# Kernel optimization log

Measured on AMD Instinct MI355X. Metric: run time of the kernel, lower is better.

Reference implementation:

```python
import math
import jax, jax.numpy as jnp
import numpy as np

B, T, D, H, L = 8, 2048, 1024, 16, 4
DK = D // H
EPS_LN = 1e-5
EPS_ATTN = 1e-6


def setup_inputs() -> dict:
    key = jax.random.key(0)
    ks = jax.random.split(key, 8)
    w = lambda k, shape: jax.random.normal(k, shape, dtype=jnp.float32) * 0.02
    return {
        'x_in': jax.random.normal(ks[0], (B, T, D), dtype=jnp.float32),
        'Wq': w(ks[1], (L, D, D)), 'bq': jnp.zeros((L, D), jnp.float32),
        'Wk': w(ks[2], (L, D, D)), 'bk': jnp.zeros((L, D), jnp.float32),
        'Wv': w(ks[3], (L, D, D)), 'bv': jnp.zeros((L, D), jnp.float32),
        'Wo': w(ks[4], (L, D, D)), 'bo': jnp.zeros((L, D), jnp.float32),
        'W1': w(ks[5], (L, D, 4 * D)), 'b1': jnp.zeros((L, 4 * D), jnp.float32),
        'W2': w(ks[6], (L, 4 * D, D)), 'b2': jnp.zeros((L, D), jnp.float32),
        'ln1_s': jnp.ones((L, D), jnp.float32), 'ln1_b': jnp.zeros((L, D), jnp.float32),
        'ln2_s': jnp.ones((L, D), jnp.float32), 'ln2_b': jnp.zeros((L, D), jnp.float32),
        'lnf_s': jnp.ones((D,), jnp.float32), 'lnf_b': jnp.zeros((D,), jnp.float32),
    }


def _layernorm(x, scale, bias):
    mu = jnp.mean(x, axis=-1, keepdims=True)
    var = jnp.mean(jnp.square(x - mu), axis=-1, keepdims=True)
    return (x - mu) * jax.lax.rsqrt(var + EPS_LN) * scale + bias


def _sinusoidal_pos_emb(t, d):
    # fairseq/MulT-style: sin half then cos half, positions start at 1 (padding_idx+1)
    half = d // 2
    freq = jnp.exp(jnp.arange(half, dtype=jnp.float32) * (-math.log(10000.0) / (half - 1)))
    pos = (jnp.arange(t, dtype=jnp.float32) + 1.0)[:, None] * freq[None, :]  # (T, half)
    return jnp.concatenate([jnp.sin(pos), jnp.cos(pos)], axis=-1)  # (T, D)


def _linear_attention(q, k, v):
    # q,k,v: (B, T, H, DK). elu+1 feature map, non-causal linear attention.
    qp = jax.nn.elu(q) + 1.0
    kp = jax.nn.elu(k) + 1.0
    kv = jnp.einsum('bshd,bshm->bhmd', kp, v)          # (B, H, DK_v, DK)
    ksum = jnp.sum(kp, axis=1)                          # (B, H, DK)
    z = 1.0 / (jnp.einsum('blhd,bhd->blh', qp, ksum) + EPS_ATTN)
    return jnp.einsum('blhd,bhmd,blh->blhm', qp, kv, z)  # (B, T, H, DK)


def _encoder_layer(x, Wq, bq, Wk, bk, Wv, bv, Wo, bo, W1, b1, W2, b2, ln1_s, ln1_b, ln2_s, ln2_b):
    b, t, d = x.shape
    # pre-LN self-attention block
    h = _layernorm(x, ln1_s, ln1_b)
    q = (h @ Wq + bq).reshape(b, t, H, DK)
    k = (h @ Wk + bk).reshape(b, t, H, DK)
    v = (h @ Wv + bv).reshape(b, t, H, DK)
    attn = _linear_attention(q, k, v).reshape(b, t, d)
    x = x + (attn @ Wo + bo)
    # pre-LN FFN block
    h = _layernorm(x, ln2_s, ln2_b)
    h = jax.nn.relu(h @ W1 + b1) @ W2 + b2
    return x + h


def reference(x_in, Wq, bq, Wk, bk, Wv, bv, Wo, bo, W1, b1, W2, b2,
              ln1_s, ln1_b, ln2_s, ln2_b, lnf_s, lnf_b):
    b, t, d = x_in.shape
    x = math.sqrt(d) * x_in + _sinusoidal_pos_emb(t, d)[None, :, :]
    for i in range(L):
        x = _encoder_layer(x, Wq[i], bq[i], Wk[i], bk[i], Wv[i], bv[i], Wo[i], bo[i],
                           W1[i], b1[i], W2[i], b2[i], ln1_s[i], ln1_b[i], ln2_s[i], ln2_b[i])
    return _layernorm(x, lnf_s, lnf_b)
```

## Files before the change

### kernel.cpp

```cpp
#include <hip/hip_runtime.h>
#include <cstdint>

#define BSZ   8
#define TSEQ  2048
#define DMOD  1024
#define NROWS 16384
#define NHEAD 16
#define DHEAD 64

__device__ __forceinline__ float bf2f(unsigned short h) {
  union { unsigned int u; float f; } a; a.u = ((unsigned int)h) << 16; return a.f;
}
__device__ __forceinline__ unsigned short f2bf(float f) {
  union { float f; unsigned int u; } a; a.f = f;
  unsigned int u = a.u;
  u += 0x7fffu + ((u >> 16) & 1u);
  return (unsigned short)(u >> 16);
}

typedef __bf16 bf16x8 __attribute__((ext_vector_type(8)));
typedef float  f32x4  __attribute__((ext_vector_type(4)));

typedef const __attribute__((address_space(1))) void* gas_ptr;
typedef __attribute__((address_space(3))) void*       las_ptr;

__device__ __forceinline__ void gl_lds16(const void* g, void* l) {
  __builtin_amdgcn_global_load_lds((gas_ptr)g, (las_ptr)l, 16, 0, 0);
}

__global__ __launch_bounds__(256) void transpose_cvt(const float* __restrict__ src,
                                                     unsigned short* __restrict__ dst,
                                                     int K, int N) {
  __shared__ float tile[32][33];
  const int n0 = blockIdx.x * 32, k0 = blockIdx.y * 32;
  const int tx = threadIdx.x, ty = threadIdx.y;
#pragma unroll
  for (int r = 0; r < 4; ++r)
    tile[ty + r * 8][tx] = src[(size_t)(k0 + ty + r * 8) * N + n0 + tx];
  __syncthreads();
#pragma unroll
  for (int r = 0; r < 4; ++r)
    dst[(size_t)(n0 + ty + r * 8) * K + k0 + tx] = f2bf(tile[tx][ty + r * 8]);
}

__global__ __launch_bounds__(256) void concat_bias(const float* __restrict__ bq,
                                                   const float* __restrict__ bk,
                                                   const float* __restrict__ bv,
                                                   float* __restrict__ out) {
  int i = blockIdx.x * 256 + threadIdx.x;
  int l = i / 3072, c = i - l * 3072;
  float v;
  if (c < 1024)       v = bq[l * 1024 + c];
  else if (c < 2048)  v = bk[l * 1024 + c - 1024];
  else                v = bv[l * 1024 + c - 2048];
  out[i] = v;
}

__global__ __launch_bounds__(256) void embed_k(const float* __restrict__ xin,
                                               float* __restrict__ x) {
  const size_t row = blockIdx.x;
  const int t = blockIdx.x & (TSEQ - 1);
  const int tid = threadIdx.x;
  const int c = tid * 4;
  float4 xv = ((const float4*)(xin + row * DMOD))[tid];
  float o[4];
  float xs[4] = { xv.x, xv.y, xv.z, xv.w };
#pragma unroll
  for (int j = 0; j < 4; ++j) {
    int dd = c + j;
    int i = dd & 511;
    float fr = expf(-0.0180241494559221f * (float)i);
    float ang = (float)(t + 1) * fr;
    float pe = (dd < 512) ? sinf(ang) : cosf(ang);
    o[j] = 32.0f * xs[j] + pe;
  }
  float4 ov = { o[0], o[1], o[2], o[3] };
  ((float4*)(x + row * DMOD))[tid] = ov;
}

__global__ __launch_bounds__(256) void ln_k(const float* __restrict__ x,
                                            const float* __restrict__ gam,
                                            const float* __restrict__ bet,
                                            unsigned short* __restrict__ outH) {
  const int row = blockIdx.x;
  const int tid = threadIdx.x;
  const float4 xv = ((const float4*)(x + (size_t)row * DMOD))[tid];
  float sum = xv.x + xv.y + xv.z + xv.w;
  float sq  = xv.x * xv.x + xv.y * xv.y + xv.z * xv.z + xv.w * xv.w;
#pragma unroll
  for (int o = 32; o; o >>= 1) { sum += __shfl_xor(sum, o); sq += __shfl_xor(sq, o); }
  __shared__ float s1[4], s2[4];
  const int wid = tid >> 6, lane = tid & 63;
  if (lane == 0) { s1[wid] = sum; s2[wid] = sq; }
  __syncthreads();
  sum = s1[0] + s1[1] + s1[2] + s1[3];
  sq  = s2[0] + s2[1] + s2[2] + s2[3];
  const float mu = sum * (1.0f / 1024.0f);
  const float var = sq * (1.0f / 1024.0f) - mu * mu;
  const float rs = rsqrtf(var + 1e-5f);
  const float4 g = ((const float4*)gam)[tid];
  const float4 b = ((const float4*)bet)[tid];
  union { unsigned short s[4]; uint2 u; } p;
  p.s[0] = f2bf((xv.x - mu) * rs * g.x + b.x);
  p.s[1] = f2bf((xv.y - mu) * rs * g.y + b.y);
  p.s[2] = f2bf((xv.z - mu) * rs * g.z + b.z);
  p.s[3] = f2bf((xv.w - mu) * rs * g.w + b.w);
  ((uint2*)(outH + (size_t)row * DMOD))[tid] = p.u;
}

template <int FINAL>
__global__ __launch_bounds__(256) void addln_k(float* __restrict__ x,
                                               const unsigned short* y,
                                               const float* __restrict__ gam,
                                               const float* __restrict__ bet,
                                               unsigned short* outH, float* outF) {
  const int row = blockIdx.x;
  const int tid = threadIdx.x;
  float4 xv = ((const float4*)(x + (size_t)row * DMOD))[tid];
  union { uint2 u; unsigned short s[4]; } yv;
  yv.u = ((const uint2*)(y + (size_t)row * DMOD))[tid];
  xv.x += bf2f(yv.s[0]); xv.y += bf2f(yv.s[1]);
  xv.z += bf2f(yv.s[2]); xv.w += bf2f(yv.s[3]);
  float sum = xv.x + xv.y + xv.z + xv.w;
  float sq  = xv.x * xv.x + xv.y * xv.y + xv.z * xv.z + xv.w * xv.w;
#pragma unroll
  for (int o = 32; o; o >>= 1) { sum += __shfl_xor(sum, o); sq += __shfl_xor(sq, o); }
  __shared__ float s1[4], s2[4];
  const int wid = tid >> 6, lane = tid & 63;
  if (lane == 0) { s1[wid] = sum; s2[wid] = sq; }
  __syncthreads();
  sum = s1[0] + s1[1] + s1[2] + s1[3];
  sq  = s2[0] + s2[1] + s2[2] + s2[3];
  const float mu = sum * (1.0f / 1024.0f);
  const float var = sq * (1.0f / 1024.0f) - mu * mu;
  const float rs = rsqrtf(var + 1e-5f);
  const float4 g = ((const float4*)gam)[tid];
  const float4 b = ((const float4*)bet)[tid];
  float o0 = (xv.x - mu) * rs * g.x + b.x;
  float o1 = (xv.y - mu) * rs * g.y + b.y;
  float o2 = (xv.z - mu) * rs * g.z + b.z;
  float o3 = (xv.w - mu) * rs * g.w + b.w;
  if (FINAL) {
    float4 ov = { o0, o1, o2, o3 };
    ((float4*)(outF + (size_t)row * DMOD))[tid] = ov;
  } else {
    ((float4*)(x + (size_t)row * DMOD))[tid] = xv;
    union { unsigned short s[4]; uint2 u; } p;
    p.s[0] = f2bf(o0); p.s[1] = f2bf(o1); p.s[2] = f2bf(o2); p.s[3] = f2bf(o3);
    ((uint2*)(outH + (size_t)row * DMOD))[tid] = p.u;
  }
}

template <int RELU>
__global__ __launch_bounds__(256) void gemm_bt(const unsigned short* __restrict__ A,
                                               const unsigned short* __restrict__ Bt,
                                               const float* __restrict__ bias,
                                               unsigned short* __restrict__ outH,
                                               int M, int N, int K, int lda) {
  __shared__ __align__(16) unsigned short sm[16384];
  unsigned short* As = sm;
  unsigned short* Bs = sm + 8192;
  const int tid = threadIdx.x;
  const int wid = tid >> 6, lane = tid & 63;
  const int wm = wid >> 1, wn = wid & 1;
  const long m0 = (long)blockIdx.x * 128, n0 = (long)blockIdx.y * 128;

  f32x4 acc[4][4] = {};

  const int srow = tid >> 3;
  const int cswz = (tid & 7) ^ (srow & 7);
  const unsigned short* Ag = A + (size_t)(m0 + srow) * lda + cswz * 8;
  const unsigned short* Bg = Bt + (size_t)(n0 + srow) * K + cswz * 8;
  char* AsW = (char*)As + wid * 1024;
  char* BsW = (char*)Bs + wid * 1024;
  const size_t a32 = (size_t)32 * lda, b32 = (size_t)32 * K;

  const int fr = lane & 15;
  const int aswz = (((lane >> 4) ^ (lane & 7)) << 4);
  const int arow = (wm * 64 + fr) << 7;
  const int brow = (wn * 64 + fr) << 7;
  const char* smc = (const char*)sm;
  const char* smcB = (const char*)(sm + 8192);

  for (int kt = 0; kt < K; kt += 64) {
    __syncthreads();
#pragma unroll
    for (int p = 0; p < 4; ++p) {
      gl_lds16(Ag + kt + (size_t)p * a32, AsW + p * 4096);
      gl_lds16(Bg + kt + (size_t)p * b32, BsW + p * 4096);
    }
    __syncthreads();
#pragma unroll
    for (int s = 0; s < 2; ++s) {
      const int offs = aswz ^ (s << 6);
      bf16x8 af[4], bfv[4];
#pragma unroll
      for (int i = 0; i < 4; ++i) {
        af[i]  = *(const bf16x8*)(smc  + arow + i * 2048 + offs);
        bfv[i] = *(const bf16x8*)(smcB + brow + i * 2048 + offs);
      }
#pragma unroll
      for (int i = 0; i < 4; ++i)
#pragma unroll
        for (int j = 0; j < 4; ++j)
          acc[i][j] = __builtin_amdgcn_mfma_f32_16x16x32_bf16(af[i], bfv[j], acc[i][j], 0, 0, 0);
    }
  }

  const int cq = lane >> 4, cn = lane & 15;
#pragma unroll
  for (int p = 0; p < 2; ++p) {
    __syncthreads();
    if (wn == p) {
#pragma unroll
      for (int i = 0; i < 4; ++i)
#pragma unroll
        for (int j = 0; j < 4; ++j) {
          const float bb = bias[n0 + p * 64 + j * 16 + cn];
#pragma unroll
          for (int v = 0; v < 4; ++v) {
            float val = acc[i][j][v] + bb;
            if (RELU) val = fmaxf(val, 0.0f);
            sm[(wm * 64 + i * 16 + cq * 4 + v) * 72 + j * 16 + cn] = f2bf(val);
          }
        }
    }
    __syncthreads();
#pragma unroll
    for (int q = 0; q < 4; ++q) {
      const int idx = q * 256 + tid;
      const int row = idx >> 3, cc = idx & 7;
      uint4 valq = *(const uint4*)(sm + row * 72 + cc * 8);
      *(uint4*)(outH + (size_t)(m0 + row) * N + n0 + p * 64 + cc * 8) = valq;
    }
  }
}

__global__ __launch_bounds__(256) void attn_kv_partial(const unsigned short* __restrict__ qkv,
                                                       float* __restrict__ kvp,
                                                       float* __restrict__ ksump) {
  const int bh = blockIdx.x, tc = blockIdx.y;
  const int b = bh >> 4, h = bh & 15;
  const int tid = threadIdx.x;
  const int m = tid & 63, wid = tid >> 6;
  __shared__ float ks[32][64];
  __shared__ float vs[32][64];
  float acc[16];
#pragma unroll
  for (int j = 0; j < 16; ++j) acc[j] = 0.0f;
  float ksacc = 0.0f;
  const int tt = tid >> 3;
  const int dsb = (tid & 7) * 8;
  const size_t base = ((size_t)b * TSEQ + tc * 256) * 3072;
  const int kcol = 1024 + h * 64 + dsb, vcol = 2048 + h * 64 + dsb;
  for (int sc = 0; sc < 8; ++sc) {
    __syncthreads();
    const size_t roff = base + (size_t)(sc * 32 + tt) * 3072;
    uint4 kb = *(const uint4*)(qkv + roff + kcol);
    uint4 vb = *(const uint4*)(qkv + roff + vcol);
    const unsigned int* kw = (const unsigned int*)&kb;
    const unsigned int* vw = (const unsigned int*)&vb;
#pragma unroll
    for (int w2 = 0; w2 < 4; ++w2) {
      float k0 = bf2f((unsigned short)(kw[w2] & 0xffffu));
      float k1 = bf2f((unsigned short)(kw[w2] >> 16));
      ks[tt][dsb + 2 * w2]     = (k0 > 0.f) ? k0 + 1.f : expf(k0);
      ks[tt][dsb + 2 * w2 + 1] = (k1 > 0.f) ? k1 + 1.f : expf(k1);
      vs[tt][dsb + 2 * w2]     = bf2f((unsigned short)(vw[w2] & 0xffffu));
      vs[tt][dsb + 2 * w2 + 1] = bf2f((unsigned short)(vw[w2] >> 16));
    }
    __syncthreads();
#pragma unroll 4
    for (int t2 = 0; t2 < 32; ++t2) {
      float vv = vs[t2][m];
#pragma unroll
      for (int j = 0; j < 16; ++j) acc[j] += ks[t2][wid * 16 + j] * vv;
      if (tid < 64) ksacc += ks[t2][tid];
    }
  }
  float* dst = kvp + (size_t)(tc * 128 + bh) * 4096;
#pragma unroll
  for (int j = 0; j < 16; ++j) dst[(wid * 16 + j) * 64 + m] = acc[j];
  if (tid < 64) ksump[(size_t)(tc * 128 + bh) * 64 + tid] = ksacc;
}

__global__ __launch_bounds__(256) void attn_kv_reduce(const float* __restrict__ kvp,
                                                      const float* __restrict__ ksump,
                                                      float* __restrict__ kvf,
                                                      float* __restrict__ ksumf) {
  const int bh = blockIdx.x;
  const int tid = threadIdx.x;
  for (int i = tid; i < 4096; i += 256) {
    float s = 0.f;
#pragma unroll
    for (int tc = 0; tc < 8; ++tc) s += kvp[(size_t)(tc * 128 + bh) * 4096 + i];
    kvf[(size_t)bh * 4096 + i] = s;
  }
  if (tid < 64) {
    float s = 0.f;
#pragma unroll
    for (int tc = 0; tc < 8; ++tc) s += ksump[(size_t)(tc * 128 + bh) * 64 + tid];
    ksumf[bh * 64 + tid] = s;
  }
}

__global__ __launch_bounds__(256) void attn_out_k(const unsigned short* __restrict__ qkv,
                                                  const float* __restrict__ kvf,
                                                  const float* __restrict__ ksumf,
                                                  unsigned short* __restrict__ qkvO) {
  const int bh = blockIdx.x, tcb = blockIdx.y;
  const int b = bh >> 4, h = bh & 15;
  const int tid = threadIdx.x, wid = tid >> 6, lane = tid & 63;
  __shared__ float kvs[4096];
  __shared__ float kss[64];
  __shared__ float qps[4][64];
  for (int i = tid; i < 1024; i += 256)
    ((float4*)kvs)[i] = ((const float4*)(kvf + (size_t)bh * 4096))[i];
  if (tid < 64) kss[tid] = ksumf[bh * 64 + tid];
  __syncthreads();
  for (int it = 0; it < 64; ++it) {
    const int t = tcb * 256 + wid * 64 + it;
    const size_t row = (size_t)b * TSEQ + t;
    float q = bf2f(qkv[row * 3072 + h * 64 + lane]);
    float qp = (q > 0.f) ? q + 1.f : expf(q);
    float r = qp * kss[lane];
#pragma unroll
    for (int o = 32; o; o >>= 1) r += __shfl_xor(r, o);
    const float z = 1.0f / (r + 1e-6f);
    qps[wid][lane] = qp;
    float o = 0.f;
#pragma unroll
    for (int d = 0; d < 64; ++d) o += qps[wid][d] * kvs[d * 64 + lane];
    qkvO[row * 3072 + h * 64 + lane] = f2bf(o * z);
  }
}

extern "C" void kernel_launch(void* const* d_in, const int* in_sizes, int n_in,
                              void* d_out, int out_size, void* d_ws, size_t ws_size,
                              hipStream_t stream) {
  const float* x_in = (const float*)d_in[0];
  const float* Wq = (const float*)d_in[1];
  const float* bq = (const float*)d_in[2];
  const float* Wk = (const float*)d_in[3];
  const float* bk = (const float*)d_in[4];
  const float* Wv = (const float*)d_in[5];
  const float* bv = (const float*)d_in[6];
  const float* Wo = (const float*)d_in[7];
  const float* bo = (const float*)d_in[8];
  const float* W1 = (const float*)d_in[9];
  const float* b1 = (const float*)d_in[10];
  const float* W2 = (const float*)d_in[11];
  const float* b2 = (const float*)d_in[12];
  const float* ln1s = (const float*)d_in[13];
  const float* ln1b = (const float*)d_in[14];
  const float* ln2s = (const float*)d_in[15];
  const float* ln2b = (const float*)d_in[16];
  const float* lnfs = (const float*)d_in[17];
  const float* lnfb = (const float*)d_in[18];

  float* x = (float*)d_out;

  char* w = (char*)d_ws;
  unsigned short* hh    = (unsigned short*)(w + 0);
  unsigned short* qkv   = (unsigned short*)(w + 33554432);
  unsigned short* h1    = (unsigned short*)(w + 33554432);
  unsigned short* qkvwt = (unsigned short*)(w + 167772160);
  unsigned short* wot   = (unsigned short*)(w + 174063616);
  unsigned short* w1t   = (unsigned short*)(w + 176160768);
  unsigned short* w2t   = (unsigned short*)(w + 184549376);
  float*          bqkv  = (float*)(w + 192937984);
  float*          kvp   = (float*)(w + 192987136);
  float*          ksump = (float*)(w + 209764352);
  float*          kvf   = (float*)(w + 210026496);
  float*          ksumf = (float*)(w + 212123648);
  (void)ws_size; (void)in_sizes; (void)n_in; (void)out_size;

  dim3 b256(256);
  dim3 tb(32, 8);
  concat_bias<<<48, b256, 0, stream>>>(bq, bk, bv, bqkv);
  embed_k<<<NROWS, b256, 0, stream>>>(x_in, x);
  ln_k<<<NROWS, b256, 0, stream>>>(x, ln1s, ln1b, hh);

  for (int l = 0; l < 4; ++l) {
    transpose_cvt<<<dim3(32, 32), tb, 0, stream>>>(Wq + (size_t)l * 1048576, qkvwt,           1024, 1024);
    transpose_cvt<<<dim3(32, 32), tb, 0, stream>>>(Wk + (size_t)l * 1048576, qkvwt + 1048576, 1024, 1024);
    transpose_cvt<<<dim3(32, 32), tb, 0, stream>>>(Wv + (size_t)l * 1048576, qkvwt + 2097152, 1024, 1024);
    transpose_cvt<<<dim3(32, 32), tb, 0, stream>>>(Wo + (size_t)l * 1048576, wot, 1024, 1024);
    transpose_cvt<<<dim3(128, 32), tb, 0, stream>>>(W1 + (size_t)l * 4194304, w1t, 1024, 4096);
    transpose_cvt<<<dim3(32, 128), tb, 0, stream>>>(W2 + (size_t)l * 4194304, w2t, 4096, 1024);

    gemm_bt<0><<<dim3(128, 24), b256, 0, stream>>>(hh, qkvwt, bqkv + l * 3072, qkv,
                                                   NROWS, 3072, 1024, 1024);
    attn_kv_partial<<<dim3(128, 8), b256, 0, stream>>>(qkv, kvp, ksump);
    attn_kv_reduce<<<128, b256, 0, stream>>>(kvp, ksump, kvf, ksumf);
    attn_out_k<<<dim3(128, 8), b256, 0, stream>>>(qkv, kvf, ksumf, qkv);
    gemm_bt<0><<<dim3(128, 8), b256, 0, stream>>>(qkv, wot, bo + l * 1024, hh,
                                                  NROWS, 1024, 1024, 3072);
    addln_k<0><<<NROWS, b256, 0, stream>>>(x, hh, ln2s + l * 1024, ln2b + l * 1024, hh, nullptr);
    gemm_bt<1><<<dim3(128, 32), b256, 0, stream>>>(hh, w1t, b1 + l * 4096, h1,
                                                   NROWS, 4096, 1024, 1024);
    gemm_bt<0><<<dim3(128, 8), b256, 0, stream>>>(h1, w2t, b2 + l * 1024, hh,
                                                  NROWS, 1024, 4096, 4096);
    if (l < 3)
      addln_k<0><<<NROWS, b256, 0, stream>>>(x, hh, ln1s + (l + 1) * 1024, ln1b + (l + 1) * 1024,
                                             hh, nullptr);
    else
      addln_k<1><<<NROWS, b256, 0, stream>>>(x, hh, lnfs, lnfb, nullptr, x);
  }
}
```

Before: 3.411 ms.

## Replace 128x128 GEMM with 256x256 double-buffered 8-wave pipelined GEMM

Rewrites the bf16 GEMM to use 256x256 output tiles with 512 threads, double-buffered LDS staging and interleaved prefetch of next tiles between MFMA phases with wave priority hints. Adds an XCD-aware workgroup remap so neighbouring tiles share cache, and a swizzled LDS epilogue for coalesced stores. The aim is to raise MFMA utilisation and cut global memory traffic per FLOP, at the cost of 128KB LDS per block and high register pressure.

```diff
diff --git a/kernel.cpp b/kernel.cpp
--- a/kernel.cpp
+++ b/kernel.cpp
@@ -152,87 +152,181 @@
 }
 
 template <int RELU>
-__global__ __launch_bounds__(256) void gemm_bt(const unsigned short* __restrict__ A,
-                                               const unsigned short* __restrict__ Bt,
-                                               const float* __restrict__ bias,
-                                               unsigned short* __restrict__ outH,
-                                               int M, int N, int K, int lda) {
-  __shared__ __align__(16) unsigned short sm[16384];
-  unsigned short* As = sm;
-  unsigned short* Bs = sm + 8192;
+__global__ __launch_bounds__(512, 2) void gemm256(const unsigned short* __restrict__ A,
+                                                  const unsigned short* __restrict__ Bt,
+                                                  const float* __restrict__ bias,
+                                                  unsigned short* __restrict__ outH,
+                                                  int M, int N, int K, int lda) {
+  __shared__ __align__(16) unsigned short sm[65536];
   const int tid = threadIdx.x;
   const int wid = tid >> 6, lane = tid & 63;
-  const int wm = wid >> 1, wn = wid & 1;
-  const long m0 = (long)blockIdx.x * 128, n0 = (long)blockIdx.y * 128;
-
-  f32x4 acc[4][4] = {};
+  const int wm = wid >> 2, wn = wid & 3;
+
+  const int nwg = gridDim.x;
+  const int q = nwg >> 3, r = nwg & 7;
+  const int xcd = blockIdx.x & 7, sub = blockIdx.x >> 3;
+  const int wg = (xcd < r ? xcd * (q + 1) : r * (q + 1) + (xcd - r) * q) + sub;
+  const int nbm = M >> 8;
+  const int bm = wg % nbm, bn = wg / nbm;
+  const long m0 = (long)bm << 8, n0 = (long)bn << 8;
 
   const int srow = tid >> 3;
   const int cswz = (tid & 7) ^ (srow & 7);
   const unsigned short* Ag = A + (size_t)(m0 + srow) * lda + cswz * 8;
   const unsigned short* Bg = Bt + (size_t)(n0 + srow) * K + cswz * 8;
-  char* AsW = (char*)As + wid * 1024;
-  char* BsW = (char*)Bs + wid * 1024;
-  const size_t a32 = (size_t)32 * lda, b32 = (size_t)32 * K;
+  char* const smb = (char*)sm;
+  const int nT = K >> 6;
+
+#define STAGE_A(t, h)                                                              \
+  do {                                                                             \
+    const unsigned short* g_ = Ag + (size_t)(t) * 64 + (size_t)((h) * 128) * lda;  \
+    char* d_ = smb + (((t) & 1) << 15) + ((h) << 14) + (wid << 10);                \
+    gl_lds16(g_, d_);                                                              \
+    gl_lds16(g_ + ((size_t)lda << 6), d_ + 8192);                                  \
+  } while (0)
+#define STAGE_B(t, h)                                                              \
+  do {                                                                             \
+    const unsigned short* g_ = Bg + (size_t)(t) * 64 + (size_t)((h) * 128) * K;    \
+    char* d_ = smb + 65536 + (((t) & 1) << 15) + ((h) << 14) + (wid << 10);        \
+    gl_lds16(g_, d_);                                                              \
+    gl_lds16(g_ + ((size_t)K << 6), d_ + 8192);                                    \
+  } while (0)
 
   const int fr = lane & 15;
-  const int aswz = (((lane >> 4) ^ (lane & 7)) << 4);
-  const int arow = (wm * 64 + fr) << 7;
-  const int brow = (wn * 64 + fr) << 7;
-  const char* smc = (const char*)sm;
-  const char* smcB = (const char*)(sm + 8192);
-
-  for (int kt = 0; kt < K; kt += 64) {
-    __syncthreads();
-#pragma unroll
-    for (int p = 0; p < 4; ++p) {
-      gl_lds16(Ag + kt + (size_t)p * a32, AsW + p * 4096);
-      gl_lds16(Bg + kt + (size_t)p * b32, BsW + p * 4096);
+  const int aswz = ((lane >> 4) ^ (lane & 7)) << 4;
+  const int aoff = (wm * 128 + fr) * 128;
+  const int boff = (wn * 64 + fr) * 128;
+
+  f32x4 acc[8][4] = {};
+  bf16x8 a0[4][2], a1[4][2], bfr[4][2];
+
+  STAGE_A(0, 0); STAGE_A(0, 1); STAGE_B(0, 0); STAGE_B(0, 1);
+  if (nT > 1) {
+    STAGE_B(1, 1); STAGE_B(1, 0); STAGE_A(1, 1);
+    asm volatile("s_waitcnt vmcnt(6)" ::: "memory");
+  } else {
+    asm volatile("s_waitcnt vmcnt(0)" ::: "memory");
+  }
+  asm volatile("s_barrier" ::: "memory");
+
+  for (int T = 0; T < nT; ++T) {
+    const char* Ab = smb + ((T & 1) << 15);
+    const char* Bb = Ab + 65536;
+
+#pragma unroll
+    for (int i = 0; i < 4; ++i)
+#pragma unroll
+      for (int ks = 0; ks < 2; ++ks) {
+        a0[i][ks]  = *(const bf16x8*)(Ab + aoff + i * 2048 + (aswz ^ (ks << 6)));
+        bfr[i][ks] = *(const bf16x8*)(Bb + boff + i * 2048 + (aswz ^ (ks << 6)));
+      }
+    if (T + 1 < nT) STAGE_A(T + 1, 0);
+    asm volatile("s_barrier" ::: "memory");
+    asm volatile("s_waitcnt lgkmcnt(0)" ::: "memory");
+    __builtin_amdgcn_sched_barrier(0);
+    __builtin_amdgcn_s_setprio(1);
+#pragma unroll
+    for (int i = 0; i < 4; ++i)
+#pragma unroll
+      for (int j = 0; j < 2; ++j)
+#pragma unroll
+        for (int ks = 0; ks < 2; ++ks)
+          acc[i][j] = __builtin_amdgcn_mfma_f32_16x16x32_bf16(a0[i][ks], bfr[j][ks], acc[i][j], 0, 0, 0);
+    __builtin_amdgcn_s_setprio(0);
+    __builtin_amdgcn_sched_barrier(0);
+    asm volatile("s_barrier" ::: "memory");
+
+#pragma unroll
+    for (int i = 0; i < 2; ++i)
+#pragma unroll
+      for (int ks = 0; ks < 2; ++ks)
+        a1[i][ks] = *(const bf16x8*)(Ab + aoff + (i + 4) * 2048 + (aswz ^ (ks << 6)));
+    if (T + 2 < nT) STAGE_B(T + 2, 1);
+    asm volatile("s_barrier" ::: "memory");
+    __builtin_amdgcn_sched_barrier(0);
+    __builtin_amdgcn_s_setprio(1);
+#pragma unroll
+    for (int i = 0; i < 4; ++i)
+#pragma unroll
+      for (int j = 2; j < 4; ++j)
+#pragma unroll
+        for (int ks = 0; ks < 2; ++ks)
+          acc[i][j] = __builtin_amdgcn_mfma_f32_16x16x32_bf16(a0[i][ks], bfr[j][ks], acc[i][j], 0, 0, 0);
+    __builtin_amdgcn_s_setprio(0);
+    __builtin_amdgcn_sched_barrier(0);
+    asm volatile("s_barrier" ::: "memory");
+
+#pragma unroll
+    for (int i = 2; i < 4; ++i)
+#pragma unroll
+      for (int ks = 0; ks < 2; ++ks)
+        a1[i][ks] = *(const bf16x8*)(Ab + aoff + (i + 4) * 2048 + (aswz ^ (ks << 6)));
+    if (T + 2 < nT) STAGE_B(T + 2, 0);
+    asm volatile("s_barrier" ::: "memory");
+    asm volatile("s_waitcnt lgkmcnt(0)" ::: "memory");
+    __builtin_amdgcn_sched_barrier(0);
+    __builtin_amdgcn_s_setprio(1);
+#pragma unroll
+    for (int i = 0; i < 4; ++i)
+#pragma unroll
+      for (int j = 0; j < 2; ++j)
+#pragma unroll
+        for (int ks = 0; ks < 2; ++ks)
+          acc[i + 4][j] = __builtin_amdgcn_mfma_f32_16x16x32_bf16(a1[i][ks], bfr[j][ks], acc[i + 4][j], 0, 0, 0);
+    __builtin_amdgcn_s_setprio(0);
+    __builtin_amdgcn_sched_barrier(0);
+    asm volatile("s_barrier" ::: "memory");
+
+    if (T + 2 < nT) {
+      STAGE_A(T + 2, 1);
+      asm volatile("s_waitcnt vmcnt(6)" ::: "memory");
+    } else {
+      asm volatile("s_waitcnt vmcnt(0)" ::: "memory");
     }
-    __syncthreads();
-#pragma unroll
-    for (int s = 0; s < 2; ++s) {
-      const int offs = aswz ^ (s << 6);
-      bf16x8 af[4], bfv[4];
-#pragma unroll
-      for (int i = 0; i < 4; ++i) {
-        af[i]  = *(const bf16x8*)(smc  + arow + i * 2048 + offs);
-        bfv[i] = *(const bf16x8*)(smcB + brow + i * 2048 + offs);
-      }
-#pragma unroll
-      for (int i = 0; i < 4; ++i)
-#pragma unroll
-        for (int j = 0; j < 4; ++j)
-          acc[i][j] = __builtin_amdgcn_mfma_f32_16x16x32_bf16(af[i], bfv[j], acc[i][j], 0, 0, 0);
-    }
-  }
-
-  const int cq = lane >> 4, cn = lane & 15;
-#pragma unroll
-  for (int p = 0; p < 2; ++p) {
-    __syncthreads();
-    if (wn == p) {
-#pragma unroll
-      for (int i = 0; i < 4; ++i)
-#pragma unroll
-        for (int j = 0; j < 4; ++j) {
-          const float bb = bias[n0 + p * 64 + j * 16 + cn];
-#pragma unroll
-          for (int v = 0; v < 4; ++v) {
-            float val = acc[i][j][v] + bb;
-            if (RELU) val = fmaxf(val, 0.0f);
-            sm[(wm * 64 + i * 16 + cq * 4 + v) * 72 + j * 16 + cn] = f2bf(val);
-          }
+    asm volatile("s_barrier" ::: "memory");
+    __builtin_amdgcn_sched_barrier(0);
+    __builtin_amdgcn_s_setprio(1);
+#pragma unroll
+    for (int i = 0; i < 4; ++i)
+#pragma unroll
+      for (int j = 2; j < 4; ++j)
+#pragma unroll
+        for (int ks = 0; ks < 2; ++ks)
+          acc[i + 4][j] = __builtin_amdgcn_mfma_f32_16x16x32_bf16(a1[i][ks], bfr[j][ks], acc[i + 4][j], 0, 0, 0);
+    __builtin_amdgcn_s_setprio(0);
+    __builtin_amdgcn_sched_barrier(0);
+    asm volatile("s_barrier" ::: "memory");
+  }
+#undef STAGE_A
+#undef STAGE_B
+
+  asm volatile("s_waitcnt vmcnt(0)" ::: "memory");
+  __syncthreads();
+  {
+    const int cq = lane >> 4, cn = lane & 15;
+#pragma unroll
+    for (int j = 0; j < 4; ++j) {
+      const float bb = bias[n0 + wn * 64 + j * 16 + cn];
+#pragma unroll
+      for (int i = 0; i < 8; ++i)
+#pragma unroll
+        for (int v = 0; v < 4; ++v) {
+          const int row = wm * 128 + i * 16 + cq * 4 + v;
+          const int col = wn * 64 + j * 16 + cn;
+          float val = acc[i][j][v] + bb;
+          if (RELU) val = fmaxf(val, 0.0f);
+          sm[row * 256 + (col ^ ((row & 12) << 2))] = f2bf(val);
         }
     }
-    __syncthreads();
-#pragma unroll
-    for (int q = 0; q < 4; ++q) {
-      const int idx = q * 256 + tid;
-      const int row = idx >> 3, cc = idx & 7;
-      uint4 valq = *(const uint4*)(sm + row * 72 + cc * 8);
-      *(uint4*)(outH + (size_t)(m0 + row) * N + n0 + p * 64 + cc * 8) = valq;
-    }
+  }
+  __syncthreads();
+#pragma unroll
+  for (int it = 0; it < 16; ++it) {
+    const int row = it * 16 + (tid >> 5);
+    const int ch = tid & 31;
+    const int chs = ch ^ ((row & 12) >> 1);
+    const uint4 val = *(const uint4*)(sm + row * 256 + chs * 8);
+    *(uint4*)(outH + (size_t)(m0 + row) * N + n0 + ch * 8) = val;
   }
 }
 
@@ -376,6 +470,7 @@
   (void)ws_size; (void)in_sizes; (void)n_in; (void)out_size;
 
   dim3 b256(256);
+  dim3 b512(512);
   dim3 tb(32, 8);
   concat_bias<<<48, b256, 0, stream>>>(bq, bk, bv, bqkv);
   embed_k<<<NROWS, b256, 0, stream>>>(x_in, x);
@@ -389,17 +484,17 @@
     transpose_cvt<<<dim3(128, 32), tb, 0, stream>>>(W1 + (size_t)l * 4194304, w1t, 1024, 4096);
     transpose_cvt<<<dim3(32, 128), tb, 0, stream>>>(W2 + (size_t)l * 4194304, w2t, 4096, 1024);
 
-    gemm_bt<0><<<dim3(128, 24), b256, 0, stream>>>(hh, qkvwt, bqkv + l * 3072, qkv,
+    gemm256<0><<<dim3(64 * 12), b512, 0, stream>>>(hh, qkvwt, bqkv + l * 3072, qkv,
                                                    NROWS, 3072, 1024, 1024);
     attn_kv_partial<<<dim3(128, 8), b256, 0, stream>>>(qkv, kvp, ksump);
     attn_kv_reduce<<<128, b256, 0, stream>>>(kvp, ksump, kvf, ksumf);
     attn_out_k<<<dim3(128, 8), b256, 0, stream>>>(qkv, kvf, ksumf, qkv);
-    gemm_bt<0><<<dim3(128, 8), b256, 0, stream>>>(qkv, wot, bo + l * 1024, hh,
+    gemm256<0><<<dim3(64 * 4), b512, 0, stream>>>(qkv, wot, bo + l * 1024, hh,
                                                   NROWS, 1024, 1024, 3072);
     addln_k<0><<<NROWS, b256, 0, stream>>>(x, hh, ln2s + l * 1024, ln2b + l * 1024, hh, nullptr);
-    gemm_bt<1><<<dim3(128, 32), b256, 0, stream>>>(hh, w1t, b1 + l * 4096, h1,
+    gemm256<1><<<dim3(64 * 16), b512, 0, stream>>>(hh, w1t, b1 + l * 4096, h1,
                                                    NROWS, 4096, 1024, 1024);
-    gemm_bt<0><<<dim3(128, 8), b256, 0, stream>>>(h1, w2t, b2 + l * 1024, hh,
+    gemm256<0><<<dim3(64 * 4), b512, 0, stream>>>(h1, w2t, b2 + l * 1024, hh,
                                                   NROWS, 1024, 4096, 4096);
     if (l < 3)
       addln_k<0><<<NROWS, b256, 0, stream>>>(x, hh, ln1s + (l + 1) * 1024, ln1b + (l + 1) * 1024,
```

Result: faster. 2.833 ms (-16.9%).
